# Kernel tuning notes

Measured on AMD Instinct MI355X. Metric: run time of the kernel, lower is better.

The kernel has to match this reference:

```python
import jax, jax.numpy as jnp
import numpy as np

N, E, F_IN, H_MID, D_OUT = 20000, 320000, 1024, 256, 128
SCALE_PARAM = 3.0
LEAKY_SLOPE = 0.01


def setup_inputs() -> dict:
    key = jax.random.key(0)
    ks = jax.random.split(key, 12)
    inv = lambda k, i, o: jax.random.normal(k, (i, o), jnp.float32) / np.sqrt(i)
    return {
        "x": jax.random.normal(ks[0], (N, F_IN), jnp.float32),
        "edge_index": jax.random.randint(ks[1], (2, E), 0, N, dtype=jnp.int64),
        "W_gcn": inv(ks[2], F_IN, H_MID),
        "b_gcn": jnp.zeros((H_MID,), jnp.float32),
        "Wq": inv(ks[3], H_MID, D_OUT), "bq": jnp.zeros((D_OUT,), jnp.float32),
        "Wk": inv(ks[4], H_MID, D_OUT), "bk": jnp.zeros((D_OUT,), jnp.float32),
        "Wv": inv(ks[5], H_MID, D_OUT), "bv": jnp.zeros((D_OUT,), jnp.float32),
        "Ws": inv(ks[6], H_MID, D_OUT), "bs": jnp.zeros((D_OUT,), jnp.float32),
    }


def reference(x, edge_index, W_gcn, b_gcn, Wq, bq, Wk, bk, Wv, bv, Ws, bs):
    n = x.shape[0]
    src, dst = edge_index[0], edge_index[1]  # message flows src(j) -> dst(i)

    # ---- GCNConv(feature_dim -> inter_dim), add_self_loops=True, sym norm ----
    loop = jnp.arange(n, dtype=src.dtype)
    row = jnp.concatenate([src, loop])
    col = jnp.concatenate([dst, loop])
    deg = jax.ops.segment_sum(jnp.ones(row.shape, x.dtype), col, num_segments=n)
    dinv = jnp.where(deg > 0, jax.lax.rsqrt(deg), 0.0)
    norm = dinv[row] * dinv[col]                      # [E+N]
    h = x @ W_gcn                                     # [N, H_MID]
    h = jax.ops.segment_sum(h[row] * norm[:, None], col, num_segments=n) + b_gcn
    h = jnp.where(h >= 0, h, LEAKY_SLOPE * h)         # LeakyReLU
    # Dropout(p) is identity at inference.

    # ---- TransformerConvReducrLayer (heads=1, no self loops, sigmoid score) ----
    d = Wq.shape[1]
    q = h @ Wq + bq
    k = h @ Wk + bk
    v = h @ Wv + bv
    alpha = jnp.sum(q[dst] * k[src], axis=-1) / jnp.sqrt(jnp.asarray(d, h.dtype))  # [E]
    alpha = alpha - alpha.mean()
    alpha = alpha / ((1.0 / SCALE_PARAM) * jnp.std(alpha, ddof=1))  # torch unbiased std
    alpha = jax.nn.sigmoid(alpha)
    msg = v[src] * alpha[:, None]                     # [E, D_OUT]
    out = jax.ops.segment_sum(msg, dst, num_segments=n)
    out = out + (h @ Ws + bs)                         # root_weight skip (PyG default)
    return out
```

## Files before the change

### kernel.cpp

```cpp
#include <hip/hip_runtime.h>
#include <hip/hip_bf16.h>

#define NNODES 20000
#define EEDGES 320000
#define FIN 1024
#define HMID 256
#define DOUT 128
#define ALPHA_BLOCKS ((NNODES + 3) / 4)

typedef __bf16 bf16x8 __attribute__((ext_vector_type(8)));
typedef __bf16 bf16x4 __attribute__((ext_vector_type(4)));
typedef __bf16 bf16x2 __attribute__((ext_vector_type(2)));
typedef float f32x4 __attribute__((ext_vector_type(4)));

typedef const __attribute__((address_space(1))) void* gas_ptr;
typedef __attribute__((address_space(3))) void* las_ptr;
__device__ __forceinline__ void async_copy16(const void* g, void* l) {
    __builtin_amdgcn_global_load_lds((gas_ptr)g, (las_ptr)l, 16, 0, 0);
}

__global__ void k_pack_w(const float* __restrict__ W, __bf16* __restrict__ Wtp) {
    int tid = blockIdx.x * 256 + threadIdx.x;
    if (tid >= FIN * HMID) return;
    int k = tid >> 8;
    int n = tid & 255;
    int kk = k >> 5, kq = (k >> 3) & 3, j = k & 7;
    int h = n >> 7;
    int u = kq * 128 + (n & 127);
    Wtp[((size_t)(kk * 2 + h) * 512 + u) * 8 + j] = (__bf16)W[tid];
}

__global__ void k_prep_watt(const float* __restrict__ Wq, const float* __restrict__ Wk,
                            const float* __restrict__ Wv, const float* __restrict__ Ws,
                            const float* __restrict__ bq, const float* __restrict__ bk,
                            const float* __restrict__ bv, const float* __restrict__ bs,
                            __bf16* __restrict__ Wallt, float* __restrict__ ball) {
    int g = blockIdx.y;
    const float* W = (g == 0) ? Wq : (g == 1) ? Wk : (g == 2) ? Wv : Ws;
    int tid = blockIdx.x * 256 + threadIdx.x;
    if (tid < HMID * DOUT) {
        int k = tid >> 7;
        int n = tid & 127;
        Wallt[(size_t)(g * DOUT + n) * HMID + k] = (__bf16)W[tid];
    }
    if (tid < DOUT) {
        const float* b = (g == 0) ? bq : (g == 1) ? bk : (g == 2) ? bv : bs;
        ball[g * DOUT + tid] = b[tid];
    }
}

__global__ void k_init(int* __restrict__ cnt, float* __restrict__ S) {
    int i = blockIdx.x * 256 + threadIdx.x;
    if (i < NNODES) cnt[i] = 0;
    if (i < 16) S[i] = 0.0f;
}

__global__ void k_count(const int* __restrict__ dst, int* __restrict__ cnt) {
    int e = blockIdx.x * 256 + threadIdx.x;
    if (e < EEDGES) atomicAdd(&cnt[dst[e]], 1);
}

__global__ void k_dinv(const int* __restrict__ cnt, float* __restrict__ dinv,
                       int* __restrict__ cursor) {
    int i = blockIdx.x * 256 + threadIdx.x;
    if (i < NNODES) {
        dinv[i] = rsqrtf((float)cnt[i] + 1.0f);
        cursor[i] = 0;
    }
}

__global__ __launch_bounds__(1024) void k_scan(const int* __restrict__ cnt,
                                               int* __restrict__ rowptr) {
    __shared__ int sh[1024];
    int t = threadIdx.x;
    int base = t * 20;
    int local[20];
    int sum = 0;
#pragma unroll
    for (int j = 0; j < 20; j++) {
        int i = base + j;
        int v = (i < NNODES) ? cnt[i] : 0;
        local[j] = sum;
        sum += v;
    }
    sh[t] = sum;
    __syncthreads();
    for (int off = 1; off < 1024; off <<= 1) {
        int v = (t >= off) ? sh[t - off] : 0;
        __syncthreads();
        sh[t] += v;
        __syncthreads();
    }
    int prev = (t > 0) ? sh[t - 1] : 0;
#pragma unroll
    for (int j = 0; j < 20; j++) {
        int i = base + j;
        if (i < NNODES) rowptr[i] = prev + local[j];
    }
    if (t == 1023) rowptr[NNODES] = sh[1023];
}

__global__ void k_fill(const int* __restrict__ src, const int* __restrict__ dst,
                       const int* __restrict__ rowptr, int* __restrict__ cursor,
                       const float* __restrict__ dinv,
                       int* __restrict__ srcsorted, float* __restrict__ wsorted) {
    int e = blockIdx.x * 256 + threadIdx.x;
    if (e >= EEDGES) return;
    int d = dst[e];
    int s = src[e];
    int pos = atomicAdd(&cursor[d], 1);
    int w = rowptr[d] + pos;
    srcsorted[w] = s;
    wsorted[w] = dinv[s];
}

__global__ __launch_bounds__(256) void k_gemm1(const float* __restrict__ x,
                                               const __bf16* __restrict__ Wtp,
                                               __bf16* __restrict__ h0bf) {
    __shared__ __bf16 As[1024];
    __shared__ __bf16 Bs[4096];
    int t = threadIdx.x;
    int lane = t & 63;
    int m = lane & 15, q = lane >> 4;
    int w = t >> 6;
    int wc = w * 32;
    int r0 = blockIdx.x * 32;
    int h = blockIdx.y;
    int c0 = h * 128;

    int arow = t >> 3;
    const float* ap = x + (size_t)(r0 + arow) * FIN + (t & 7) * 4;
    __bf16* awr = &As[arow * 32 + ((t & 7) >> 1) * 8 + (t & 1) * 4];
    const __bf16* bb = Wtp + (size_t)h * 4096;

    f32x4 acc[2][2] = {};

    float4 a = *(const float4*)(ap);

#pragma unroll 1
    for (int kk = 0; kk < 32; kk++) {
        async_copy16(bb + (size_t)kk * 8192 + t * 8, &Bs[t * 8]);
        async_copy16(bb + (size_t)kk * 8192 + (t + 256) * 8, &Bs[(t + 256) * 8]);
        bf16x4 av;
        av[0] = (__bf16)a.x; av[1] = (__bf16)a.y; av[2] = (__bf16)a.z; av[3] = (__bf16)a.w;
        *(bf16x4*)awr = av;
        if (kk + 1 < 32) a = *(const float4*)(ap + (kk + 1) * 32);
        __syncthreads();

        bf16x8 af[2], bfr[2];
#pragma unroll
        for (int i = 0; i < 2; i++)
            af[i] = *(const bf16x8*)&As[(i * 16 + m) * 32 + q * 8];
#pragma unroll
        for (int jb = 0; jb < 2; jb++)
            bfr[jb] = *(const bf16x8*)&Bs[(q * 128 + wc + jb * 16 + m) * 8];
#pragma unroll
        for (int i = 0; i < 2; i++)
#pragma unroll
            for (int jb = 0; jb < 2; jb++)
                acc[i][jb] = __builtin_amdgcn_mfma_f32_16x16x32_bf16(af[i], bfr[jb], acc[i][jb], 0, 0, 0);
        __syncthreads();
    }

#pragma unroll
    for (int i = 0; i < 2; i++)
#pragma unroll
        for (int jb = 0; jb < 2; jb++)
#pragma unroll
            for (int r = 0; r < 4; r++) {
                int row = r0 + i * 16 + q * 4 + r;
                int col = c0 + wc + jb * 16 + m;
                h0bf[(size_t)row * 256 + col] = (__bf16)acc[i][jb][r];
            }
}

__global__ __launch_bounds__(256) void k_gcn_gather(const int* __restrict__ rowptr,
                                                    const int* __restrict__ srcsorted,
                                                    const float* __restrict__ wsorted,
                                                    const __bf16* __restrict__ h0bf,
                                                    const float* __restrict__ dinv,
                                                    const float* __restrict__ bgcn,
                                                    __bf16* __restrict__ hbf) {
    int gid = blockIdx.x * 256 + threadIdx.x;
    int n = gid >> 6, l = gid & 63;
    if (n >= NNODES) return;
    float dn = dinv[n];
    float wn = dn * dn;
    bf16x4 hv = *(const bf16x4*)(h0bf + (size_t)n * 256 + l * 4);
    float4 b = ((const float4*)bgcn)[l];
    float ax = (float)hv[0] * wn + b.x;
    float ay = (float)hv[1] * wn + b.y;
    float az = (float)hv[2] * wn + b.z;
    float aw = (float)hv[3] * wn + b.w;
    int beg = rowptr[n], end = rowptr[n + 1];
    for (int i = beg; i < end; i += 4) {
        int i1 = i + 1 < end ? i + 1 : end - 1;
        int i2 = i + 2 < end ? i + 2 : end - 1;
        int i3 = i + 3 < end ? i + 3 : end - 1;
        int s0 = srcsorted[i], s1 = srcsorted[i1], s2 = srcsorted[i2], s3 = srcsorted[i3];
        float w0 = wsorted[i] * dn;
        float w1 = (i + 1 < end) ? wsorted[i1] * dn : 0.f;
        float w2 = (i + 2 < end) ? wsorted[i2] * dn : 0.f;
        float w3 = (i + 3 < end) ? wsorted[i3] * dn : 0.f;
        bf16x4 v0 = *(const bf16x4*)(h0bf + (size_t)s0 * 256 + l * 4);
        bf16x4 v1 = *(const bf16x4*)(h0bf + (size_t)s1 * 256 + l * 4);
        bf16x4 v2 = *(const bf16x4*)(h0bf + (size_t)s2 * 256 + l * 4);
        bf16x4 v3 = *(const bf16x4*)(h0bf + (size_t)s3 * 256 + l * 4);
        ax += (float)v0[0] * w0 + (float)v1[0] * w1 + (float)v2[0] * w2 + (float)v3[0] * w3;
        ay += (float)v0[1] * w0 + (float)v1[1] * w1 + (float)v2[1] * w2 + (float)v3[1] * w3;
        az += (float)v0[2] * w0 + (float)v1[2] * w1 + (float)v2[2] * w2 + (float)v3[2] * w3;
        aw += (float)v0[3] * w0 + (float)v1[3] * w1 + (float)v2[3] * w2 + (float)v3[3] * w3;
    }
    bf16x4 o;
    o[0] = (__bf16)(ax >= 0.f ? ax : 0.01f * ax);
    o[1] = (__bf16)(ay >= 0.f ? ay : 0.01f * ay);
    o[2] = (__bf16)(az >= 0.f ? az : 0.01f * az);
    o[3] = (__bf16)(aw >= 0.f ? aw : 0.01f * aw);
    *(bf16x4*)(hbf + (size_t)n * 256 + l * 4) = o;
}

__global__ __launch_bounds__(256) void k_gemm2(const __bf16* __restrict__ hbf,
                                               const __bf16* __restrict__ Wallt,
                                               const float* __restrict__ ball,
                                               __bf16* __restrict__ qarr,
                                               __bf16* __restrict__ karr,
                                               __bf16* __restrict__ varr,
                                               __bf16* __restrict__ sarr) {
    __shared__ __bf16 As[4096];
    __shared__ __bf16 Bs[4096];
    int t = threadIdx.x;
    int lane = t & 63;
    int m = lane & 15, q = lane >> 4;
    int wave = t >> 6;
    int wr = (wave & 1) * 64;
    int wc = (wave >> 1) * 64;
    int r0 = blockIdx.x * 128;
    int c0 = blockIdx.y * 128;
    __bf16* tbl = (blockIdx.y == 0) ? qarr : (blockIdx.y == 1) ? karr
                : (blockIdx.y == 2) ? varr : sarr;

    const __bf16* asrc[2];
    __bf16* aldst[2];
#pragma unroll
    for (int j = 0; j < 2; j++) {
        int u = j * 256 + t;
        int row = r0 + (u & 127);
        if (row >= NNODES) row = NNODES - 1;
        asrc[j] = hbf + (size_t)row * HMID + (u >> 7) * 8;
        aldst[j] = &As[(size_t)u * 8];
    }
    const __bf16* bsrc[2];
    __bf16* bldst[2];
#pragma unroll
    for (int j = 0; j < 2; j++) {
        int u = j * 256 + t;
        bsrc[j] = Wallt + (size_t)(c0 + (u & 127)) * HMID + (u >> 7) * 8;
        bldst[j] = &Bs[(size_t)u * 8];
    }

    f32x4 acc[4][4] = {};

    for (int k0 = 0; k0 < HMID; k0 += 32) {
#pragma unroll
        for (int j = 0; j < 2; j++) async_copy16(asrc[j] + k0, aldst[j]);
#pragma unroll
        for (int j = 0; j < 2; j++) async_copy16(bsrc[j] + k0, bldst[j]);
        __syncthreads();

        bf16x8 af[4], bfr[4];
#pragma unroll
        for (int i = 0; i < 4; i++) af[i] = *(const bf16x8*)&As[(size_t)(q * 128 + wr + i * 16 + m) * 8];
#pragma unroll
        for (int jb = 0; jb < 4; jb++) bfr[jb] = *(const bf16x8*)&Bs[(size_t)(q * 128 + wc + jb * 16 + m) * 8];
#pragma unroll
        for (int i = 0; i < 4; i++)
#pragma unroll
            for (int jb = 0; jb < 4; jb++)
                acc[i][jb] = __builtin_amdgcn_mfma_f32_16x16x32_bf16(af[i], bfr[jb], acc[i][jb], 0, 0, 0);
        __syncthreads();
    }

#pragma unroll
    for (int jb = 0; jb < 4; jb++) {
        int dcol = wc + jb * 16 + m;
        float bias = ball[c0 + dcol];
#pragma unroll
        for (int i = 0; i < 4; i++)
#pragma unroll
            for (int r = 0; r < 4; r++) {
                int row = r0 + wr + i * 16 + q * 4 + r;
                if (row < NNODES) tbl[(size_t)row * 128 + dcol] = (__bf16)(acc[i][jb][r] + bias);
            }
    }
}

__global__ __launch_bounds__(256) void k_alpha(const int* __restrict__ rowptr,
                                               const int* __restrict__ srcsorted,
                                               const __bf16* __restrict__ qarr,
                                               const __bf16* __restrict__ karr,
                                               float* __restrict__ alpha,
                                               float* __restrict__ part) {
    int n = (blockIdx.x * 256 + threadIdx.x) >> 6;
    int lane = threadIdx.x & 63;
    int g = lane >> 4, l = lane & 15;
    float s1 = 0.f, s2 = 0.f;
    if (n < NNODES) {
        bf16x8 qb = *(const bf16x8*)(qarr + (size_t)n * 128 + l * 8);
        float qf[8];
#pragma unroll
        for (int j = 0; j < 8; j++) qf[j] = (float)qb[j];
        int beg = rowptr[n], end = rowptr[n + 1];
        for (int i = beg + g; i < end; i += 16) {
            int i1 = i + 4 < end ? i + 4 : end - 1;
            int i2 = i + 8 < end ? i + 8 : end - 1;
            int i3 = i + 12 < end ? i + 12 : end - 1;
            int s0 = srcsorted[i], sA = srcsorted[i1], sB = srcsorted[i2], sC = srcsorted[i3];
            bf16x8 k0 = *(const bf16x8*)(karr + (size_t)s0 * 128 + l * 8);
            bf16x8 k1 = *(const bf16x8*)(karr + (size_t)sA * 128 + l * 8);
            bf16x8 k2 = *(const bf16x8*)(karr + (size_t)sB * 128 + l * 8);
            bf16x8 k3 = *(const bf16x8*)(karr + (size_t)sC * 128 + l * 8);
            float d0 = 0.f, d1 = 0.f, d2 = 0.f, d3 = 0.f;
#pragma unroll
            for (int j = 0; j < 8; j++) {
                d0 += qf[j] * (float)k0[j];
                d1 += qf[j] * (float)k1[j];
                d2 += qf[j] * (float)k2[j];
                d3 += qf[j] * (float)k3[j];
            }
#pragma unroll
            for (int off = 1; off < 16; off <<= 1) {
                d0 += __shfl_xor(d0, off, 64);
                d1 += __shfl_xor(d1, off, 64);
                d2 += __shfl_xor(d2, off, 64);
                d3 += __shfl_xor(d3, off, 64);
            }
            if (l == 0) {
                const float sc = 0.08838834764831845f;
                float a0 = d0 * sc;
                alpha[i] = a0; s1 += a0; s2 += a0 * a0;
                if (i + 4 < end)  { float a = d1 * sc; alpha[i + 4]  = a; s1 += a; s2 += a * a; }
                if (i + 8 < end)  { float a = d2 * sc; alpha[i + 8]  = a; s1 += a; s2 += a * a; }
                if (i + 12 < end) { float a = d3 * sc; alpha[i + 12] = a; s1 += a; s2 += a * a; }
            }
        }
    }
#pragma unroll
    for (int off = 1; off < 64; off <<= 1) {
        s1 += __shfl_xor(s1, off, 64);
        s2 += __shfl_xor(s2, off, 64);
    }
    __shared__ float sh[8];
    int wave = threadIdx.x >> 6;
    if ((threadIdx.x & 63) == 0) { sh[wave] = s1; sh[4 + wave] = s2; }
    __syncthreads();
    if (threadIdx.x == 0) {
        part[2 * blockIdx.x]     = sh[0] + sh[1] + sh[2] + sh[3];
        part[2 * blockIdx.x + 1] = sh[4] + sh[5] + sh[6] + sh[7];
    }
}

__global__ __launch_bounds__(1024) void k_stats(const float* __restrict__ part,
                                                float* __restrict__ S) {
    float s1 = 0.f, s2 = 0.f;
    for (int i = threadIdx.x; i < ALPHA_BLOCKS; i += 1024) {
        s1 += part[2 * i];
        s2 += part[2 * i + 1];
    }
#pragma unroll
    for (int off = 1; off < 64; off <<= 1) {
        s1 += __shfl_xor(s1, off, 64);
        s2 += __shfl_xor(s2, off, 64);
    }
    __shared__ float sh1[16], sh2[16];
    int wave = threadIdx.x >> 6;
    if ((threadIdx.x & 63) == 0) { sh1[wave] = s1; sh2[wave] = s2; }
    __syncthreads();
    if (threadIdx.x == 0) {
        float t1 = 0.f, t2 = 0.f;
#pragma unroll
        for (int w = 0; w < 16; w++) { t1 += sh1[w]; t2 += sh2[w]; }
        float mean = t1 / (float)EEDGES;
        float var = (t2 - (float)EEDGES * mean * mean) / (float)(EEDGES - 1);
        float stdv = sqrtf(fmaxf(var, 1e-20f));
        S[2] = mean;
        S[3] = 3.0f / stdv;
    }
}

__global__ __launch_bounds__(256) void k_msg_gather(const int* __restrict__ rowptr,
                                                    const int* __restrict__ srcsorted,
                                                    const __bf16* __restrict__ varr,
                                                    const __bf16* __restrict__ sarr,
                                                    const float* __restrict__ alpha,
                                                    const float* __restrict__ S,
                                                    float* __restrict__ out) {
    int n = (blockIdx.x * 256 + threadIdx.x) >> 6;
    int l = threadIdx.x & 63;
    if (n >= NNODES) return;
    float mean = S[2], scl = S[3];
    bf16x2 sb = *(const bf16x2*)(sarr + (size_t)n * 128 + l * 2);
    float ax = (float)sb[0], ay = (float)sb[1];
    int beg = rowptr[n], end = rowptr[n + 1];
    for (int i = beg; i < end; i += 4) {
        int i1 = i + 1 < end ? i + 1 : end - 1;
        int i2 = i + 2 < end ? i + 2 : end - 1;
        int i3 = i + 3 < end ? i + 3 : end - 1;
        int s0 = srcsorted[i], s1 = srcsorted[i1], s2 = srcsorted[i2], s3 = srcsorted[i3];
        float z0 = (alpha[i] - mean) * scl;
        float z1 = (alpha[i1] - mean) * scl;
        float z2 = (alpha[i2] - mean) * scl;
        float z3 = (alpha[i3] - mean) * scl;
        float g0 = 1.0f / (1.0f + __expf(-z0));
        float g1 = (i + 1 < end) ? 1.0f / (1.0f + __expf(-z1)) : 0.f;
        float g2 = (i + 2 < end) ? 1.0f / (1.0f + __expf(-z2)) : 0.f;
        float g3 = (i + 3 < end) ? 1.0f / (1.0f + __expf(-z3)) : 0.f;
        bf16x2 v0 = *(const bf16x2*)(varr + (size_t)s0 * 128 + l * 2);
        bf16x2 v1 = *(const bf16x2*)(varr + (size_t)s1 * 128 + l * 2);
        bf16x2 v2 = *(const bf16x2*)(varr + (size_t)s2 * 128 + l * 2);
        bf16x2 v3 = *(const bf16x2*)(varr + (size_t)s3 * 128 + l * 2);
        ax += (float)v0[0] * g0 + (float)v1[0] * g1 + (float)v2[0] * g2 + (float)v3[0] * g3;
        ay += (float)v0[1] * g0 + (float)v1[1] * g1 + (float)v2[1] * g2 + (float)v3[1] * g3;
    }
    float2 o; o.x = ax; o.y = ay;
    ((float2*)(out + (size_t)n * DOUT))[l] = o;
}

extern "C" void kernel_launch(void* const* d_in, const int* in_sizes, int n_in,
                              void* d_out, int out_size, void* d_ws, size_t ws_size,
                              hipStream_t stream) {
    const float* x  = (const float*)d_in[0];
    const int* ei   = (const int*)d_in[1];
    const int* srcI = ei;
    const int* dstI = ei + EEDGES;
    const float* Wg = (const float*)d_in[2];
    const float* bg = (const float*)d_in[3];
    const float* Wq = (const float*)d_in[4];  const float* bq = (const float*)d_in[5];
    const float* Wk = (const float*)d_in[6];  const float* bk = (const float*)d_in[7];
    const float* Wv = (const float*)d_in[8];  const float* bv = (const float*)d_in[9];
    const float* Ws = (const float*)d_in[10]; const float* bs = (const float*)d_in[11];
    float* out = (float*)d_out;

    char* wsb = (char*)d_ws;
    size_t off = 0;
    auto alloc = [&](size_t bytes) -> void* {
        void* p = wsb + off;
        off += (bytes + 255) & ~(size_t)255;
        return p;
    };
    int*    cnt    = (int*)alloc((size_t)NNODES * 4);
    int*    rowptr = (int*)alloc((size_t)(NNODES + 1) * 4);
    int*    cursor = (int*)alloc((size_t)NNODES * 4);
    int*    srcst  = (int*)alloc((size_t)EEDGES * 4);
    float*  wsort  = (float*)alloc((size_t)EEDGES * 4);
    float*  dinv   = (float*)alloc((size_t)NNODES * 4);
    float*  S      = (float*)alloc(64);
    float*  part   = (float*)alloc((size_t)ALPHA_BLOCKS * 2 * 4);
    __bf16* Wtp    = (__bf16*)alloc((size_t)32 * 8192 * 2);
    __bf16* Wallt  = (__bf16*)alloc((size_t)512 * HMID * 2);
    float*  ball   = (float*)alloc(512 * 4);
    __bf16* h0bf   = (__bf16*)alloc((size_t)NNODES * HMID * 2);
    __bf16* hbf    = (__bf16*)alloc((size_t)NNODES * HMID * 2);
    __bf16* qarr   = (__bf16*)alloc((size_t)NNODES * 128 * 2);
    __bf16* karr   = (__bf16*)alloc((size_t)NNODES * 128 * 2);
    __bf16* varr   = (__bf16*)alloc((size_t)NNODES * 128 * 2);
    __bf16* sarr   = (__bf16*)alloc((size_t)NNODES * 128 * 2);
    float*  alphab = (float*)alloc((size_t)EEDGES * 4);
    if (off > ws_size) return;

    k_pack_w<<<(FIN * HMID + 255) / 256, 256, 0, stream>>>(Wg, Wtp);
    dim3 gw((HMID * DOUT + 255) / 256, 4);
    k_prep_watt<<<gw, 256, 0, stream>>>(Wq, Wk, Wv, Ws, bq, bk, bv, bs, Wallt, ball);

    k_init<<<(NNODES + 255) / 256, 256, 0, stream>>>(cnt, S);
    k_count<<<(EEDGES + 255) / 256, 256, 0, stream>>>(dstI, cnt);
    k_dinv<<<(NNODES + 255) / 256, 256, 0, stream>>>(cnt, dinv, cursor);
    k_scan<<<1, 1024, 0, stream>>>(cnt, rowptr);
    k_fill<<<(EEDGES + 255) / 256, 256, 0, stream>>>(srcI, dstI, rowptr, cursor, dinv, srcst, wsort);

    dim3 g1(625, 2);
    k_gemm1<<<g1, 256, 0, stream>>>(x, Wtp, h0bf);

    k_gcn_gather<<<(NNODES * 64 + 255) / 256, 256, 0, stream>>>(rowptr, srcst, wsort, h0bf, dinv, bg, hbf);

    dim3 g2((NNODES + 127) / 128, 4);
    k_gemm2<<<g2, 256, 0, stream>>>(hbf, Wallt, ball, qarr, karr, varr, sarr);

    k_alpha<<<ALPHA_BLOCKS, 256, 0, stream>>>(rowptr, srcst, qarr, karr, alphab, part);
    k_stats<<<1, 1024, 0, stream>>>(part, S);

    k_msg_gather<<<(NNODES * 64 + 255) / 256, 256, 0, stream>>>(rowptr, srcst, varr, sarr, alphab, S, out);
}
```

Measured before the change: 313.3 us.

## Retile gemm1 to 16-row blocks with 64-wide K steps and swizzled A tile

```diff
diff --git a/kernel.cpp b/kernel.cpp
--- a/kernel.cpp
+++ b/kernel.cpp
@@ -118,60 +118,64 @@
                                                const __bf16* __restrict__ Wtp,
                                                __bf16* __restrict__ h0bf) {
     __shared__ __bf16 As[1024];
-    __shared__ __bf16 Bs[4096];
+    __shared__ __bf16 Bs[8192];
     int t = threadIdx.x;
     int lane = t & 63;
     int m = lane & 15, q = lane >> 4;
     int w = t >> 6;
     int wc = w * 32;
-    int r0 = blockIdx.x * 32;
+    int r0 = blockIdx.x * 16;
     int h = blockIdx.y;
     int c0 = h * 128;
 
-    int arow = t >> 3;
-    const float* ap = x + (size_t)(r0 + arow) * FIN + (t & 7) * 4;
-    __bf16* awr = &As[arow * 32 + ((t & 7) >> 1) * 8 + (t & 1) * 4];
+    int arow = t >> 4;
+    const float* ap = x + (size_t)(r0 + arow) * FIN + (t & 15) * 4;
+    int ku = (t & 15) >> 1;
+    __bf16* awr = &As[(ku * 128 + arow * 8 + (t & 1) * 4) ^ (ku << 4)];
     const __bf16* bb = Wtp + (size_t)h * 4096;
 
-    f32x4 acc[2][2] = {};
+    f32x4 acc[2] = {};
 
     float4 a = *(const float4*)(ap);
 
 #pragma unroll 1
-    for (int kk = 0; kk < 32; kk++) {
-        async_copy16(bb + (size_t)kk * 8192 + t * 8, &Bs[t * 8]);
-        async_copy16(bb + (size_t)kk * 8192 + (t + 256) * 8, &Bs[(t + 256) * 8]);
+    for (int kk = 0; kk < 16; kk++) {
+        const __bf16* bsrc = bb + (size_t)kk * 16384;
+        async_copy16(bsrc + t * 8, &Bs[t * 8]);
+        async_copy16(bsrc + (t + 256) * 8, &Bs[(t + 256) * 8]);
+        async_copy16(bsrc + 8192 + t * 8, &Bs[4096 + t * 8]);
+        async_copy16(bsrc + 8192 + (t + 256) * 8, &Bs[4096 + (t + 256) * 8]);
         bf16x4 av;
         av[0] = (__bf16)a.x; av[1] = (__bf16)a.y; av[2] = (__bf16)a.z; av[3] = (__bf16)a.w;
         *(bf16x4*)awr = av;
-        if (kk + 1 < 32) a = *(const float4*)(ap + (kk + 1) * 32);
-        __syncthreads();
-
-        bf16x8 af[2], bfr[2];
-#pragma unroll
-        for (int i = 0; i < 2; i++)
-            af[i] = *(const bf16x8*)&As[(i * 16 + m) * 32 + q * 8];
-#pragma unroll
-        for (int jb = 0; jb < 2; jb++)
-            bfr[jb] = *(const bf16x8*)&Bs[(q * 128 + wc + jb * 16 + m) * 8];
-#pragma unroll
-        for (int i = 0; i < 2; i++)
+        if (kk + 1 < 16) a = *(const float4*)(ap + (kk + 1) * 64);
+        __syncthreads();
+
+        bf16x8 af[2], bfr[2][2];
+#pragma unroll
+        for (int s = 0; s < 2; s++) {
+            int kb = s * 4 + q;
+            af[s] = *(const bf16x8*)&As[(kb * 128 + m * 8) ^ (kb << 4)];
 #pragma unroll
             for (int jb = 0; jb < 2; jb++)
-                acc[i][jb] = __builtin_amdgcn_mfma_f32_16x16x32_bf16(af[i], bfr[jb], acc[i][jb], 0, 0, 0);
-        __syncthreads();
-    }
-
-#pragma unroll
-    for (int i = 0; i < 2; i++)
-#pragma unroll
-        for (int jb = 0; jb < 2; jb++)
-#pragma unroll
-            for (int r = 0; r < 4; r++) {
-                int row = r0 + i * 16 + q * 4 + r;
-                int col = c0 + wc + jb * 16 + m;
-                h0bf[(size_t)row * 256 + col] = (__bf16)acc[i][jb][r];
-            }
+                bfr[s][jb] = *(const bf16x8*)&Bs[s * 4096 + (q * 128 + wc + jb * 16 + m) * 8];
+        }
+#pragma unroll
+        for (int s = 0; s < 2; s++)
+#pragma unroll
+            for (int jb = 0; jb < 2; jb++)
+                acc[jb] = __builtin_amdgcn_mfma_f32_16x16x32_bf16(af[s], bfr[s][jb], acc[jb], 0, 0, 0);
+        __syncthreads();
+    }
+
+#pragma unroll
+    for (int jb = 0; jb < 2; jb++)
+#pragma unroll
+        for (int r = 0; r < 4; r++) {
+            int row = r0 + q * 4 + r;
+            int col = c0 + wc + jb * 16 + m;
+            h0bf[(size_t)row * 256 + col] = (__bf16)acc[jb][r];
+        }
 }
 
 __global__ __launch_bounds__(256) void k_gcn_gather(const int* __restrict__ rowptr,
@@ -477,7 +481,7 @@
     k_scan<<<1, 1024, 0, stream>>>(cnt, rowptr);
     k_fill<<<(EEDGES + 255) / 256, 256, 0, stream>>>(srcI, dstI, rowptr, cursor, dinv, srcst, wsort);
 
-    dim3 g1(625, 2);
+    dim3 g1(1250, 2);
     k_gemm1<<<g1, 256, 0, stream>>>(x, Wtp, h0bf);
 
     k_gcn_gather<<<(NNODES * 64 + 255) / 256, 256, 0, stream>>>(rowptr, srcst, wsort, h0bf, dinv, bg, hbf);
```

Measured after the change: 329.7 us. 1.05x slower.

## Triple-buffer GEMM1 tiles with async fp32 A loads and swizzled LDS layout

Applied to the files above, without the earlier changes.

```diff
diff --git a/kernel.cpp b/kernel.cpp
--- a/kernel.cpp
+++ b/kernel.cpp
@@ -117,8 +117,8 @@
 __global__ __launch_bounds__(256) void k_gemm1(const float* __restrict__ x,
                                                const __bf16* __restrict__ Wtp,
                                                __bf16* __restrict__ h0bf) {
-    __shared__ __bf16 As[1024];
-    __shared__ __bf16 Bs[4096];
+    __shared__ float  Af[3][1024];
+    __shared__ __bf16 Bsb[3][4096];
     int t = threadIdx.x;
     int lane = t & 63;
     int m = lane & 15, q = lane >> 4;
@@ -129,37 +129,54 @@
     int c0 = h * 128;
 
     int arow = t >> 3;
-    const float* ap = x + (size_t)(r0 + arow) * FIN + (t & 7) * 4;
-    __bf16* awr = &As[arow * 32 + ((t & 7) >> 1) * 8 + (t & 1) * 4];
+    int ag = ((t & 7) - arow) & 7;
+    const float* ap = x + (size_t)(r0 + arow) * FIN + ag * 4;
     const __bf16* bb = Wtp + (size_t)h * 4096;
 
     f32x4 acc[2][2] = {};
 
-    float4 a = *(const float4*)(ap);
+    auto stage = [&](int buf, int kk) {
+        async_copy16(ap + kk * 32, &Af[buf][t * 4]);
+        const __bf16* bsrc = bb + (size_t)kk * 8192;
+        async_copy16(bsrc + t * 8, &Bsb[buf][t * 8]);
+        async_copy16(bsrc + (t + 256) * 8, &Bsb[buf][(t + 256) * 8]);
+    };
+
+    stage(0, 0);
+    stage(1, 1);
 
 #pragma unroll 1
     for (int kk = 0; kk < 32; kk++) {
-        async_copy16(bb + (size_t)kk * 8192 + t * 8, &Bs[t * 8]);
-        async_copy16(bb + (size_t)kk * 8192 + (t + 256) * 8, &Bs[(t + 256) * 8]);
-        bf16x4 av;
-        av[0] = (__bf16)a.x; av[1] = (__bf16)a.y; av[2] = (__bf16)a.z; av[3] = (__bf16)a.w;
-        *(bf16x4*)awr = av;
-        if (kk + 1 < 32) a = *(const float4*)(ap + (kk + 1) * 32);
-        __syncthreads();
-
+        int b = kk % 3;
+        if (kk + 2 < 32) stage((kk + 2) % 3, kk + 2);
+        if (kk < 30)       asm volatile("s_waitcnt vmcnt(6)\ns_barrier" ::: "memory");
+        else if (kk == 30) asm volatile("s_waitcnt vmcnt(3)\ns_barrier" ::: "memory");
+        else               asm volatile("s_waitcnt vmcnt(0)\ns_barrier" ::: "memory");
+
+        const float*  A_ = Af[b];
+        const __bf16* B_ = Bsb[b];
         bf16x8 af[2], bfr[2];
 #pragma unroll
-        for (int i = 0; i < 2; i++)
-            af[i] = *(const bf16x8*)&As[(i * 16 + m) * 32 + q * 8];
+        for (int i = 0; i < 2; i++) {
+            int r = i * 16 + m;
+            int p0 = (2 * q + r) & 7;
+            int p1 = (2 * q + 1 + r) & 7;
+            f32x4 u0 = *(const f32x4*)&A_[r * 32 + p0 * 4];
+            f32x4 u1 = *(const f32x4*)&A_[r * 32 + p1 * 4];
+            bf16x8 v;
+            v[0] = (__bf16)u0[0]; v[1] = (__bf16)u0[1]; v[2] = (__bf16)u0[2]; v[3] = (__bf16)u0[3];
+            v[4] = (__bf16)u1[0]; v[5] = (__bf16)u1[1]; v[6] = (__bf16)u1[2]; v[7] = (__bf16)u1[3];
+            af[i] = v;
+        }
 #pragma unroll
         for (int jb = 0; jb < 2; jb++)
-            bfr[jb] = *(const bf16x8*)&Bs[(q * 128 + wc + jb * 16 + m) * 8];
+            bfr[jb] = *(const bf16x8*)&B_[(q * 128 + wc + jb * 16 + m) * 8];
 #pragma unroll
         for (int i = 0; i < 2; i++)
 #pragma unroll
             for (int jb = 0; jb < 2; jb++)
                 acc[i][jb] = __builtin_amdgcn_mfma_f32_16x16x32_bf16(af[i], bfr[jb], acc[i][jb], 0, 0, 0);
-        __syncthreads();
+        asm volatile("s_barrier" ::: "memory");
     }
 
 #pragma unroll
```

Result: slower. 329.6 us (+5.2%).

## Drop LDS staging in both GEMMs and double-buffer operands in registers

Applied to the files above, without the earlier changes.

```diff
diff --git a/kernel.cpp b/kernel.cpp
--- a/kernel.cpp
+++ b/kernel.cpp
@@ -12,12 +12,6 @@
 typedef __bf16 bf16x4 __attribute__((ext_vector_type(4)));
 typedef __bf16 bf16x2 __attribute__((ext_vector_type(2)));
 typedef float f32x4 __attribute__((ext_vector_type(4)));
-
-typedef const __attribute__((address_space(1))) void* gas_ptr;
-typedef __attribute__((address_space(3))) void* las_ptr;
-__device__ __forceinline__ void async_copy16(const void* g, void* l) {
-    __builtin_amdgcn_global_load_lds((gas_ptr)g, (las_ptr)l, 16, 0, 0);
-}
 
 __global__ void k_pack_w(const float* __restrict__ W, __bf16* __restrict__ Wtp) {
     int tid = blockIdx.x * 256 + threadIdx.x;
@@ -114,11 +108,34 @@
     wsorted[w] = dinv[s];
 }
 
-__global__ __launch_bounds__(256) void k_gemm1(const float* __restrict__ x,
-                                               const __bf16* __restrict__ Wtp,
-                                               __bf16* __restrict__ h0bf) {
-    __shared__ __bf16 As[1024];
-    __shared__ __bf16 Bs[4096];
+#define G1_LOAD(A0L, A0H, A1L, A1H, B0, B1, KK) do {                          \
+    const float* _a0 = a0p + (KK) * 32;                                       \
+    const float* _a1 = a1p + (KK) * 32;                                       \
+    A0L = *(const float4*)_a0;  A0H = *(const float4*)(_a0 + 4);              \
+    A1L = *(const float4*)_a1;  A1H = *(const float4*)(_a1 + 4);              \
+    const __bf16* _b = bp + (size_t)(KK) * 8192;                              \
+    B0 = *(const bf16x8*)_b;  B1 = *(const bf16x8*)(_b + 128);                \
+} while (0)
+
+#define G1_COMP(A0L, A0H, A1L, A1H, B0, B1) do {                              \
+    bf16x8 _af0, _af1;                                                        \
+    _af0[0] = (__bf16)A0L.x; _af0[1] = (__bf16)A0L.y;                         \
+    _af0[2] = (__bf16)A0L.z; _af0[3] = (__bf16)A0L.w;                         \
+    _af0[4] = (__bf16)A0H.x; _af0[5] = (__bf16)A0H.y;                         \
+    _af0[6] = (__bf16)A0H.z; _af0[7] = (__bf16)A0H.w;                         \
+    _af1[0] = (__bf16)A1L.x; _af1[1] = (__bf16)A1L.y;                         \
+    _af1[2] = (__bf16)A1L.z; _af1[3] = (__bf16)A1L.w;                         \
+    _af1[4] = (__bf16)A1H.x; _af1[5] = (__bf16)A1H.y;                         \
+    _af1[6] = (__bf16)A1H.z; _af1[7] = (__bf16)A1H.w;                         \
+    acc[0][0] = __builtin_amdgcn_mfma_f32_16x16x32_bf16(_af0, B0, acc[0][0], 0, 0, 0); \
+    acc[0][1] = __builtin_amdgcn_mfma_f32_16x16x32_bf16(_af0, B1, acc[0][1], 0, 0, 0); \
+    acc[1][0] = __builtin_amdgcn_mfma_f32_16x16x32_bf16(_af1, B0, acc[1][0], 0, 0, 0); \
+    acc[1][1] = __builtin_amdgcn_mfma_f32_16x16x32_bf16(_af1, B1, acc[1][1], 0, 0, 0); \
+} while (0)
+
+__global__ __launch_bounds__(256, 3) void k_gemm1(const float* __restrict__ x,
+                                                  const __bf16* __restrict__ Wtp,
+                                                  __bf16* __restrict__ h0bf) {
     int t = threadIdx.x;
     int lane = t & 63;
     int m = lane & 15, q = lane >> 4;
@@ -128,38 +145,24 @@
     int h = blockIdx.y;
     int c0 = h * 128;
 
-    int arow = t >> 3;
-    const float* ap = x + (size_t)(r0 + arow) * FIN + (t & 7) * 4;
-    __bf16* awr = &As[arow * 32 + ((t & 7) >> 1) * 8 + (t & 1) * 4];
-    const __bf16* bb = Wtp + (size_t)h * 4096;
+    const float* a0p = x + (size_t)(r0 + m) * FIN + q * 8;
+    const float* a1p = x + (size_t)(r0 + 16 + m) * FIN + q * 8;
+    const __bf16* bp = Wtp + ((size_t)h * 512 + q * 128 + wc + m) * 8;
 
     f32x4 acc[2][2] = {};
 
-    float4 a = *(const float4*)(ap);
+    float4 pa0l, pa0h, pa1l, pa1h;  bf16x8 pb0, pb1;
+    float4 qa0l, qa0h, qa1l, qa1h;  bf16x8 qb0, qb1;
+
+    G1_LOAD(pa0l, pa0h, pa1l, pa1h, pb0, pb1, 0);
 
 #pragma unroll 1
-    for (int kk = 0; kk < 32; kk++) {
-        async_copy16(bb + (size_t)kk * 8192 + t * 8, &Bs[t * 8]);
-        async_copy16(bb + (size_t)kk * 8192 + (t + 256) * 8, &Bs[(t + 256) * 8]);
-        bf16x4 av;
-        av[0] = (__bf16)a.x; av[1] = (__bf16)a.y; av[2] = (__bf16)a.z; av[3] = (__bf16)a.w;
-        *(bf16x4*)awr = av;
-        if (kk + 1 < 32) a = *(const float4*)(ap + (kk + 1) * 32);
-        __syncthreads();
-
-        bf16x8 af[2], bfr[2];
-#pragma unroll
-        for (int i = 0; i < 2; i++)
-            af[i] = *(const bf16x8*)&As[(i * 16 + m) * 32 + q * 8];
-#pragma unroll
-        for (int jb = 0; jb < 2; jb++)
-            bfr[jb] = *(const bf16x8*)&Bs[(q * 128 + wc + jb * 16 + m) * 8];
-#pragma unroll
-        for (int i = 0; i < 2; i++)
-#pragma unroll
-            for (int jb = 0; jb < 2; jb++)
-                acc[i][jb] = __builtin_amdgcn_mfma_f32_16x16x32_bf16(af[i], bfr[jb], acc[i][jb], 0, 0, 0);
-        __syncthreads();
+    for (int kk = 0; kk < 32; kk += 2) {
+        G1_LOAD(qa0l, qa0h, qa1l, qa1h, qb0, qb1, kk + 1);
+        G1_COMP(pa0l, pa0h, pa1l, pa1h, pb0, pb1);
+        int kn = (kk + 2 < 32) ? kk + 2 : 30;
+        G1_LOAD(pa0l, pa0h, pa1l, pa1h, pb0, pb1, kn);
+        G1_COMP(qa0l, qa0h, qa1l, qa1h, qb0, qb1);
     }
 
 #pragma unroll
@@ -219,15 +222,43 @@
     *(bf16x4*)(hbf + (size_t)n * 256 + l * 4) = o;
 }
 
-__global__ __launch_bounds__(256) void k_gemm2(const __bf16* __restrict__ hbf,
-                                               const __bf16* __restrict__ Wallt,
-                                               const float* __restrict__ ball,
-                                               __bf16* __restrict__ qarr,
-                                               __bf16* __restrict__ karr,
-                                               __bf16* __restrict__ varr,
-                                               __bf16* __restrict__ sarr) {
-    __shared__ __bf16 As[4096];
-    __shared__ __bf16 Bs[4096];
+#define G2_LOAD(PA, PB, K0) do {                                              \
+    PA##0 = *(const bf16x8*)(ap0 + (K0));                                     \
+    PA##1 = *(const bf16x8*)(ap1 + (K0));                                     \
+    PA##2 = *(const bf16x8*)(ap2 + (K0));                                     \
+    PA##3 = *(const bf16x8*)(ap3 + (K0));                                     \
+    PB##0 = *(const bf16x8*)(bp0 + (K0));                                     \
+    PB##1 = *(const bf16x8*)(bp1 + (K0));                                     \
+    PB##2 = *(const bf16x8*)(bp2 + (K0));                                     \
+    PB##3 = *(const bf16x8*)(bp3 + (K0));                                     \
+} while (0)
+
+#define G2_COMP(PA, PB) do {                                                  \
+    acc[0][0] = __builtin_amdgcn_mfma_f32_16x16x32_bf16(PA##0, PB##0, acc[0][0], 0, 0, 0); \
+    acc[0][1] = __builtin_amdgcn_mfma_f32_16x16x32_bf16(PA##0, PB##1, acc[0][1], 0, 0, 0); \
+    acc[0][2] = __builtin_amdgcn_mfma_f32_16x16x32_bf16(PA##0, PB##2, acc[0][2], 0, 0, 0); \
+    acc[0][3] = __builtin_amdgcn_mfma_f32_16x16x32_bf16(PA##0, PB##3, acc[0][3], 0, 0, 0); \
+    acc[1][0] = __builtin_amdgcn_mfma_f32_16x16x32_bf16(PA##1, PB##0, acc[1][0], 0, 0, 0); \
+    acc[1][1] = __builtin_amdgcn_mfma_f32_16x16x32_bf16(PA##1, PB##1, acc[1][1], 0, 0, 0); \
+    acc[1][2] = __builtin_amdgcn_mfma_f32_16x16x32_bf16(PA##1, PB##2, acc[1][2], 0, 0, 0); \
+    acc[1][3] = __builtin_amdgcn_mfma_f32_16x16x32_bf16(PA##1, PB##3, acc[1][3], 0, 0, 0); \
+    acc[2][0] = __builtin_amdgcn_mfma_f32_16x16x32_bf16(PA##2, PB##0, acc[2][0], 0, 0, 0); \
+    acc[2][1] = __builtin_amdgcn_mfma_f32_16x16x32_bf16(PA##2, PB##1, acc[2][1], 0, 0, 0); \
+    acc[2][2] = __builtin_amdgcn_mfma_f32_16x16x32_bf16(PA##2, PB##2, acc[2][2], 0, 0, 0); \
+    acc[2][3] = __builtin_amdgcn_mfma_f32_16x16x32_bf16(PA##2, PB##3, acc[2][3], 0, 0, 0); \
+    acc[3][0] = __builtin_amdgcn_mfma_f32_16x16x32_bf16(PA##3, PB##0, acc[3][0], 0, 0, 0); \
+    acc[3][1] = __builtin_amdgcn_mfma_f32_16x16x32_bf16(PA##3, PB##1, acc[3][1], 0, 0, 0); \
+    acc[3][2] = __builtin_amdgcn_mfma_f32_16x16x32_bf16(PA##3, PB##2, acc[3][2], 0, 0, 0); \
+    acc[3][3] = __builtin_amdgcn_mfma_f32_16x16x32_bf16(PA##3, PB##3, acc[3][3], 0, 0, 0); \
+} while (0)
+
+__global__ __launch_bounds__(256, 2) void k_gemm2(const __bf16* __restrict__ hbf,
+                                                  const __bf16* __restrict__ Wallt,
+                                                  const float* __restrict__ ball,
+                                                  __bf16* __restrict__ qarr,
+                                                  __bf16* __restrict__ karr,
+                                                  __bf16* __restrict__ varr,
+                                                  __bf16* __restrict__ sarr) {
     int t = threadIdx.x;
     int lane = t & 63;
     int m = lane & 15, q = lane >> 4;
@@ -239,45 +270,35 @@
     __bf16* tbl = (blockIdx.y == 0) ? qarr : (blockIdx.y == 1) ? karr
                 : (blockIdx.y == 2) ? varr : sarr;
 
-    const __bf16* asrc[2];
-    __bf16* aldst[2];
-#pragma unroll
-    for (int j = 0; j < 2; j++) {
-        int u = j * 256 + t;
-        int row = r0 + (u & 127);
-        if (row >= NNODES) row = NNODES - 1;
-        asrc[j] = hbf + (size_t)row * HMID + (u >> 7) * 8;
-        aldst[j] = &As[(size_t)u * 8];
-    }
-    const __bf16* bsrc[2];
-    __bf16* bldst[2];
-#pragma unroll
-    for (int j = 0; j < 2; j++) {
-        int u = j * 256 + t;
-        bsrc[j] = Wallt + (size_t)(c0 + (u & 127)) * HMID + (u >> 7) * 8;
-        bldst[j] = &Bs[(size_t)u * 8];
-    }
+    int rows[4];
+#pragma unroll
+    for (int i = 0; i < 4; i++) {
+        int row = r0 + wr + i * 16 + m;
+        rows[i] = (row < NNODES) ? row : NNODES - 1;
+    }
+    const __bf16* ap0 = hbf + (size_t)rows[0] * HMID + q * 8;
+    const __bf16* ap1 = hbf + (size_t)rows[1] * HMID + q * 8;
+    const __bf16* ap2 = hbf + (size_t)rows[2] * HMID + q * 8;
+    const __bf16* ap3 = hbf + (size_t)rows[3] * HMID + q * 8;
+    const __bf16* bp0 = Wallt + (size_t)(c0 + wc +  0 + m) * HMID + q * 8;
+    const __bf16* bp1 = Wallt + (size_t)(c0 + wc + 16 + m) * HMID + q * 8;
+    const __bf16* bp2 = Wallt + (size_t)(c0 + wc + 32 + m) * HMID + q * 8;
+    const __bf16* bp3 = Wallt + (size_t)(c0 + wc + 48 + m) * HMID + q * 8;
 
     f32x4 acc[4][4] = {};
 
-    for (int k0 = 0; k0 < HMID; k0 += 32) {
-#pragma unroll
-        for (int j = 0; j < 2; j++) async_copy16(asrc[j] + k0, aldst[j]);
-#pragma unroll
-        for (int j = 0; j < 2; j++) async_copy16(bsrc[j] + k0, bldst[j]);
-        __syncthreads();
-
-        bf16x8 af[4], bfr[4];
-#pragma unroll
-        for (int i = 0; i < 4; i++) af[i] = *(const bf16x8*)&As[(size_t)(q * 128 + wr + i * 16 + m) * 8];
-#pragma unroll
-        for (int jb = 0; jb < 4; jb++) bfr[jb] = *(const bf16x8*)&Bs[(size_t)(q * 128 + wc + jb * 16 + m) * 8];
-#pragma unroll
-        for (int i = 0; i < 4; i++)
-#pragma unroll
-            for (int jb = 0; jb < 4; jb++)
-                acc[i][jb] = __builtin_amdgcn_mfma_f32_16x16x32_bf16(af[i], bfr[jb], acc[i][jb], 0, 0, 0);
-        __syncthreads();
+    bf16x8 pa0, pa1, pa2, pa3, pb0, pb1, pb2, pb3;
+    bf16x8 qa0, qa1, qa2, qa3, qb0, qb1, qb2, qb3;
+
+    G2_LOAD(pa, pb, 0);
+
+#pragma unroll 1
+    for (int k0 = 0; k0 < HMID; k0 += 64) {
+        G2_LOAD(qa, qb, k0 + 32);
+        G2_COMP(pa, pb);
+        int kn = (k0 + 64 < HMID) ? k0 + 64 : HMID - 64;
+        G2_LOAD(pa, pb, kn);
+        G2_COMP(qa, qb);
     }
 
 #pragma unroll
```

Result: slower. 366.3 us (+16.9%).
